# Kernel tuning notes

Measured on AMD Instinct MI355X. Metric: run time of the kernel, lower is better.

## Reference

```python
import jax, jax.numpy as jnp
import numpy as np

TOL = 1e-4
MAX_ITER = 50


def _newton_fixed_point(W, x):
    """Solve z = tanh(z @ W.T + x) by Newton's method (batched).

    W: [U, U], x: [B, U]. Returns (out=tanh(z*@W.T+x), z*).
    """
    B, U = x.shape
    I = jnp.eye(U, dtype=x.dtype)

    def cond(carry):
        _, it, err = carry
        return (it < MAX_ITER) & (err >= TOL)

    def body(carry):
        z, it, _ = carry
        z_lin = z @ W.T + x                      # [B, U]
        g = z - jnp.tanh(z_lin)                  # residual
        err = jnp.linalg.norm(g)                 # global Frobenius norm (as torch.norm)
        sech2 = 1.0 / jnp.cosh(z_lin) ** 2       # [B, U]
        J = I[None, :, :] - sech2[:, :, None] * W[None, :, :]  # [B, U, U]
        dz = jnp.linalg.solve(J, g[:, :, None])[:, :, 0]
        # torch breaks BEFORE the update when err < tol; emulate with where
        z_new = jnp.where(err < TOL, z, z - dz)
        return (z_new, it + 1, err)

    z0 = jnp.tanh(x)
    init = (z0, jnp.array(0, jnp.int32), jnp.array(jnp.inf, x.dtype))
    z_star, _, _ = jax.lax.while_loop(cond, body, init)
    out = jnp.tanh(z_star @ W.T + x)
    return out, z_star


def setup_inputs() -> dict:
    key = jax.random.key(0)
    ks = jax.random.split(key, 6)
    B, D_IN, U, D_OUT, L = 2048, 784, 128, 10, 2
    x = jax.random.normal(ks[0], (B, D_IN), dtype=jnp.float32)
    Wi = jax.random.normal(ks[1], (U, D_IN), dtype=jnp.float32) * (1.0 / np.sqrt(D_IN))
    bi = jax.random.normal(ks[2], (U,), dtype=jnp.float32) * 0.01
    # contractive block weights (like nn.Linear init scale) so Newton converges
    Wb = jax.random.normal(ks[3], (L, U, U), dtype=jnp.float32) * (0.5 / np.sqrt(U))
    Wo = jax.random.normal(ks[4], (D_OUT, U), dtype=jnp.float32) * (1.0 / np.sqrt(U))
    bo = jax.random.normal(ks[5], (D_OUT,), dtype=jnp.float32) * 0.01
    return {"x": x, "Wi": Wi, "bi": bi, "Wb": Wb, "Wo": Wo, "bo": bo}


def reference(x, Wi, bi, Wb, Wo, bo):
    z = x @ Wi.T + bi                              # input linear
    for l in range(Wb.shape[0]):                   # implicit Newton blocks
        z, _ = _newton_fixed_point(Wb[l], z)
    logits = z @ Wo.T + bo                         # output linear
    return jax.nn.softmax(logits, axis=1)
```

## Files before the change

### kernel.cpp

```cpp
#include <hip/hip_runtime.h>
#include <math.h>

#define U 128
#define NIT 10

typedef __attribute__((ext_vector_type(8))) short bf16x8;
typedef __attribute__((ext_vector_type(4))) float f32x4;
typedef __attribute__((ext_vector_type(4))) unsigned int u32x4;

__device__ inline unsigned int pack2(float a, float b) {
    return (__float_as_uint(a) >> 16) | (__float_as_uint(b) & 0xFFFF0000u);
}
__device__ inline float lo_of(float a) {
    return a - __uint_as_float(__float_as_uint(a) & 0xFFFF0000u);
}
__device__ inline unsigned int packrn(float a, float b) {
    unsigned int r;
    asm("v_cvt_pk_bf16_f32 %0, %1, %2" : "=v"(r) : "v"(a), "v"(b));
    return r;
}
__device__ inline float fromhi(unsigned short h) {
    return __uint_as_float(((unsigned int)h) << 16);
}
__device__ inline float rcp_fast(float x) {
    float r;
    asm("v_rcp_f32 %0, %1" : "=v"(r) : "v"(x));
    return r;
}
__device__ inline float tanh_fast(float v) {
    float e = __expf(2.0f * v);
    return __builtin_fmaf(-2.0f, rcp_fast(e + 1.0f), 1.0f);
}
#define MFMA(A, B, C) __builtin_amdgcn_mfma_f32_16x16x32_bf16(A, B, C, 0, 0, 0)

#define SPLIT8(P4, Q4, H, LO)                                              \
{   u32x4 h_, l_;                                                          \
    h_[0] = pack2(P4.x, P4.y); h_[1] = pack2(P4.z, P4.w);                  \
    h_[2] = pack2(Q4.x, Q4.y); h_[3] = pack2(Q4.z, Q4.w);                  \
    l_[0] = pack2(lo_of(P4.x), lo_of(P4.y));                               \
    l_[1] = pack2(lo_of(P4.z), lo_of(P4.w));                               \
    l_[2] = pack2(lo_of(Q4.x), lo_of(Q4.y));                               \
    l_[3] = pack2(lo_of(Q4.z), lo_of(Q4.w));                               \
    H  = __builtin_bit_cast(bf16x8, h_);                                   \
    LO = __builtin_bit_cast(bf16x8, l_); }

__global__ __launch_bounds__(512) void k_gemm_in(
        const float* __restrict__ X, const float* __restrict__ Wi,
        const float* __restrict__ bi, float* __restrict__ zA) {
    __shared__ f32x4 redS[4][64];
    const int tid  = threadIdx.x;
    const int w    = tid >> 6;
    const int lane = tid & 63;
    const int l15  = lane & 15;
    const int lq   = lane >> 4;
    const int slab = blockIdx.x & 127;
    const int ch   = blockIdx.x >> 7;
    const int ct   = w & 3;
    const int kh   = w >> 2;
    const int r0   = slab * 16;
    const int cb   = ch * 64 + ct * 16;
    const int colA = cb + l15;
    const int KD   = 784;

    const float* xp = &X[(long)(r0 + l15) * KD];
    const float* wp = &Wi[(long)colA * KD];

    f32x4 a0 = {0.f, 0.f, 0.f, 0.f};
    f32x4 a1 = {0.f, 0.f, 0.f, 0.f};
    f32x4 a2 = {0.f, 0.f, 0.f, 0.f};
    if (kh == 0) {
        float4 b4 = *(const float4*)&bi[cb + lq * 4];
        a0[0] = b4.x; a0[1] = b4.y; a0[2] = b4.z; a0[3] = b4.w;
    }

    const int kbase = kh ? 384 : 0;
    #pragma unroll 6
    for (int c = 0; c < 12; ++c) {
        const int k = kbase + c * 32 + lq * 8;
        float4 xa = *(const float4*)&xp[k];
        float4 xb = *(const float4*)&xp[k + 4];
        float4 wa = *(const float4*)&wp[k];
        float4 wb = *(const float4*)&wp[k + 4];
        bf16x8 ah, al, bh, bl;
        SPLIT8(xa, xb, ah, al)
        SPLIT8(wa, wb, bh, bl)
        a0 = MFMA(bh, ah, a0);
        a1 = MFMA(bh, al, a1);
        a2 = MFMA(bl, ah, a2);
    }
    if (kh) {
        float4 z4 = make_float4(0.f, 0.f, 0.f, 0.f);
        float4 xa = z4, xb = z4, wa = z4, wb = z4;
        if (lq < 2) {
            const int k = 768 + lq * 8;
            xa = *(const float4*)&xp[k];
            xb = *(const float4*)&xp[k + 4];
            wa = *(const float4*)&wp[k];
            wb = *(const float4*)&wp[k + 4];
        }
        bf16x8 ah, al, bh, bl;
        SPLIT8(xa, xb, ah, al)
        SPLIT8(wa, wb, bh, bl)
        a0 = MFMA(bh, ah, a0);
        a1 = MFMA(bh, al, a1);
        a2 = MFMA(bl, ah, a2);
    }

    f32x4 r;
    #pragma unroll
    for (int i = 0; i < 4; ++i) r[i] = a0[i] + a1[i] + a2[i];

    if (kh) redS[ct][lane] = r;
    __syncthreads();
    if (!kh) {
        f32x4 o = redS[ct][lane];
        float4 st;
        st.x = r[0] + o[0]; st.y = r[1] + o[1];
        st.z = r[2] + o[2]; st.w = r[3] + o[3];
        *(float4*)&zA[(long)(r0 + l15) * U + cb + lq * 4] = st;
    }
}

__global__ __launch_bounds__(256) void k_picard(
        const float* __restrict__ zA, const float* __restrict__ Wb,
        const float* __restrict__ Wo, const float* __restrict__ bo,
        float* __restrict__ Out, int L) {
    __shared__ unsigned short zhS[2][16 * U];

    const int tid  = threadIdx.x;
    const int w    = tid >> 6;
    const int lane = tid & 63;
    const int l15  = lane & 15;
    const int lq   = lane >> 4;
    const int r0   = blockIdx.x * 16;

    float xf[8], zr[8];
    {
        const float* zrow = &zA[(long)(r0 + l15) * U + w * 32 + lq * 4];
        float4 x40 = *(const float4*)&zrow[0];
        float4 x41 = *(const float4*)&zrow[16];
        xf[0] = x40.x; xf[1] = x40.y; xf[2] = x40.z; xf[3] = x40.w;
        xf[4] = x41.x; xf[5] = x41.y; xf[6] = x41.z; xf[7] = x41.w;
    }

    const int swz = (l15 & 7) << 4;
    int offA[4];
    #pragma unroll
    for (int ks = 0; ks < 4; ++ks)
        offA[ks] = l15 * 256 + ((64 * ks + 16 * lq) ^ swz);
    const int offW0 = l15 * 256 + (((64 * w + 8 * lq)) ^ swz);
    const int offW1 = l15 * 256 + (((64 * w + 32 + 8 * lq)) ^ swz);

    char* zhB = (char*)&zhS[0][0];

    for (int l = 0; l < L; ++l) {
        bf16x8 whf[2][4];
        #pragma unroll
        for (int ct = 0; ct < 2; ++ct) {
            const int colA = w * 32 + ct * 16 + l15;
            const float* wrow = &Wb[((long)l * U + colA) * U];
            #pragma unroll
            for (int ks = 0; ks < 4; ++ks) {
                const int k = ks * 32 + lq * 8;
                float4 p = *(const float4*)&wrow[k];
                float4 q = *(const float4*)&wrow[k + 4];
                u32x4 h;
                h[0] = packrn(p.x, p.y); h[1] = packrn(p.z, p.w);
                h[2] = packrn(q.x, q.y); h[3] = packrn(q.z, q.w);
                whf[ct][ks] = __builtin_bit_cast(bf16x8, h);
            }
        }

        {
            uint2 h0, h1;
            #pragma unroll
            for (int i = 0; i < 8; ++i) zr[i] = tanh_fast(xf[i]);
            h0.x = packrn(zr[0], zr[1]); h0.y = packrn(zr[2], zr[3]);
            h1.x = packrn(zr[4], zr[5]); h1.y = packrn(zr[6], zr[7]);
            *(uint2*)(zhB + offW0) = h0;
            *(uint2*)(zhB + offW1) = h1;
        }
        __syncthreads();

        #pragma unroll 2
        for (int it = 0; it < NIT; ++it) {
            const int cur = it & 1;
            const int nxt = cur ^ 1;
            bf16x8 zhf[4];
            #pragma unroll
            for (int ks = 0; ks < 4; ++ks)
                zhf[ks] = *(const bf16x8*)(zhB + cur * 4096 + offA[ks]);

            f32x4 A0 = {xf[0], xf[1], xf[2], xf[3]};
            f32x4 Z4 = {0.f, 0.f, 0.f, 0.f};
            f32x4 A1 = Z4;
            f32x4 B0 = {xf[4], xf[5], xf[6], xf[7]};
            f32x4 B1 = Z4;
            A0 = MFMA(whf[0][0], zhf[0], A0);
            B0 = MFMA(whf[1][0], zhf[0], B0);
            A1 = MFMA(whf[0][2], zhf[2], A1);
            B1 = MFMA(whf[1][2], zhf[2], B1);
            A0 = MFMA(whf[0][1], zhf[1], A0);
            B0 = MFMA(whf[1][1], zhf[1], B0);
            A1 = MFMA(whf[0][3], zhf[3], A1);
            B1 = MFMA(whf[1][3], zhf[3], B1);

            #pragma unroll
            for (int i = 0; i < 4; ++i) {
                zr[i]     = tanh_fast(A0[i] + A1[i]);
                zr[4 + i] = tanh_fast(B0[i] + B1[i]);
            }
            uint2 h0, h1;
            h0.x = packrn(zr[0], zr[1]); h0.y = packrn(zr[2], zr[3]);
            h1.x = packrn(zr[4], zr[5]); h1.y = packrn(zr[6], zr[7]);
            *(uint2*)(zhB + nxt * 4096 + offW0) = h0;
            *(uint2*)(zhB + nxt * 4096 + offW1) = h1;
            __syncthreads();
        }

        {
            bf16x8 zhf[4];
            #pragma unroll
            for (int ks = 0; ks < 4; ++ks)
                zhf[ks] = *(const bf16x8*)(zhB + offA[ks]);
            #pragma unroll
            for (int ct = 0; ct < 2; ++ct) {
                const int colA = w * 32 + ct * 16 + l15;
                const float* wrow = &Wb[((long)l * U + colA) * U];
                f32x4 dH = {xf[ct * 4 + 0], xf[ct * 4 + 1],
                            xf[ct * 4 + 2], xf[ct * 4 + 3]};
                f32x4 dL = {0.f, 0.f, 0.f, 0.f};
                #pragma unroll
                for (int ks = 0; ks < 4; ++ks) {
                    const float* wp = &wrow[32 * ks + 8 * lq];
                    float4 p = *(const float4*)&wp[0];
                    float4 q = *(const float4*)&wp[4];
                    u32x4 h = __builtin_bit_cast(u32x4, whf[ct][ks]);
                    float lo0 = p.x - __uint_as_float(h[0] << 16);
                    float lo1 = p.y - __uint_as_float(h[0] & 0xFFFF0000u);
                    float lo2 = p.z - __uint_as_float(h[1] << 16);
                    float lo3 = p.w - __uint_as_float(h[1] & 0xFFFF0000u);
                    float lo4 = q.x - __uint_as_float(h[2] << 16);
                    float lo5 = q.y - __uint_as_float(h[2] & 0xFFFF0000u);
                    float lo6 = q.z - __uint_as_float(h[3] << 16);
                    float lo7 = q.w - __uint_as_float(h[3] & 0xFFFF0000u);
                    u32x4 lw;
                    lw[0] = packrn(lo0, lo1); lw[1] = packrn(lo2, lo3);
                    lw[2] = packrn(lo4, lo5); lw[3] = packrn(lo6, lo7);
                    bf16x8 wlf = __builtin_bit_cast(bf16x8, lw);
                    dH = MFMA(whf[ct][ks], zhf[ks], dH);
                    dL = MFMA(wlf, zhf[ks], dL);
                }
                #pragma unroll
                for (int i = 0; i < 4; ++i)
                    xf[ct * 4 + i] = tanh_fast(dH[i] + dL[i]);
            }
        }
        __syncthreads();
    }

    {
        unsigned int h0 = packrn(xf[0], xf[1]);
        unsigned int h1 = packrn(xf[2], xf[3]);
        unsigned int h2 = packrn(xf[4], xf[5]);
        unsigned int h3 = packrn(xf[6], xf[7]);
        uint2 H0, H1, L0, L1;
        H0.x = h0; H0.y = h1; H1.x = h2; H1.y = h3;
        L0.x = packrn(xf[0] - __uint_as_float(h0 << 16),
                      xf[1] - __uint_as_float(h0 & 0xFFFF0000u));
        L0.y = packrn(xf[2] - __uint_as_float(h1 << 16),
                      xf[3] - __uint_as_float(h1 & 0xFFFF0000u));
        L1.x = packrn(xf[4] - __uint_as_float(h2 << 16),
                      xf[5] - __uint_as_float(h2 & 0xFFFF0000u));
        L1.y = packrn(xf[6] - __uint_as_float(h3 << 16),
                      xf[7] - __uint_as_float(h3 & 0xFFFF0000u));
        *(uint2*)(zhB + offW0) = H0;
        *(uint2*)(zhB + offW1) = H1;
        *(uint2*)(zhB + 4096 + offW0) = L0;
        *(uint2*)(zhB + 4096 + offW1) = L1;
    }
    __syncthreads();

    if (w == 0) {
        bf16x8 woh[4], wol[4];
        #pragma unroll
        for (int ks = 0; ks < 4; ++ks) {
            float4 p = make_float4(0.f, 0.f, 0.f, 0.f), q = p;
            if (l15 < 10) {
                const float* worow = &Wo[l15 * U + ks * 32 + lq * 8];
                p = *(const float4*)&worow[0];
                q = *(const float4*)&worow[4];
            }
            SPLIT8(p, q, woh[ks], wol[ks])
        }
        bf16x8 zf[4], zl[4];
        #pragma unroll
        for (int ks = 0; ks < 4; ++ks) {
            zf[ks] = *(const bf16x8*)(zhB + offA[ks]);
            zl[ks] = *(const bf16x8*)(zhB + 4096 + offA[ks]);
        }

        f32x4 d0 = {0.f, 0.f, 0.f, 0.f};
        f32x4 d1 = d0, d2 = d0;
        #pragma unroll
        for (int ks = 0; ks < 4; ++ks) {
            d0 = MFMA(woh[ks], zf[ks], d0);
            d1 = MFMA(wol[ks], zf[ks], d1);
            d2 = MFMA(woh[ks], zl[ks], d2);
        }
        float lg[4];
        #pragma unroll
        for (int i = 0; i < 4; ++i) {
            const int c = 4 * lq + i;
            lg[i] = (c < 10) ? (d0[i] + d1[i] + d2[i] + bo[c]) : -1e30f;
        }
        float m = fmaxf(fmaxf(lg[0], lg[1]), fmaxf(lg[2], lg[3]));
        m = fmaxf(m, __shfl_xor(m, 16));
        m = fmaxf(m, __shfl_xor(m, 32));
        float e[4], s = 0.f;
        #pragma unroll
        for (int i = 0; i < 4; ++i) { e[i] = __expf(lg[i] - m); s += e[i]; }
        s += __shfl_xor(s, 16);
        s += __shfl_xor(s, 32);
        const float inv = rcp_fast(s);
        const float inv2 = inv * (2.0f - s * inv);
        #pragma unroll
        for (int i = 0; i < 4; ++i) {
            const int c = 4 * lq + i;
            if (c < 10) Out[(long)(r0 + l15) * 10 + c] = e[i] * inv2;
        }
    }
}

extern "C" void kernel_launch(void* const* d_in, const int* in_sizes, int n_in,
                              void* d_out, int out_size, void* d_ws, size_t ws_size,
                              hipStream_t stream) {
    const float* x  = (const float*)d_in[0];
    const float* Wi = (const float*)d_in[1];
    const float* bi = (const float*)d_in[2];
    const float* Wb = (const float*)d_in[3];
    const float* Wo = (const float*)d_in[4];
    const float* bo = (const float*)d_in[5];
    float* out = (float*)d_out;

    const int DIN = 784;
    const int B   = in_sizes[0] / DIN;
    const int L   = in_sizes[3] / (U * U);

    float* zA = (float*)d_ws;

    k_gemm_in<<<256, 512, 0, stream>>>(x, Wi, bi, zA);
    k_picard<<<B / 16, 256, 0, stream>>>(zA, Wb, Wo, bo, out, L);
}
```

Baseline: 31.08 us.

## Process two 16-row batch tiles per block to reuse weight fragments

Each k_picard block now handles 32 batch rows as two independent 16-row tiles. The bf16 weight fragments loaded into registers and the per-iteration barriers are shared across both tiles, and the two independent MFMA chains can interleave. This halves the grid to 64 blocks. On a GPU with many CUs that means fewer active CUs, so per-block latency roughly doubles while total weight loading drops.

Result: slower. 36.81 us (+18.4%).

```diff
diff --git a/kernel.cpp b/kernel.cpp
--- a/kernel.cpp
+++ b/kernel.cpp
@@ -18,9 +18,6 @@
     unsigned int r;
     asm("v_cvt_pk_bf16_f32 %0, %1, %2" : "=v"(r) : "v"(a), "v"(b));
     return r;
-}
-__device__ inline float fromhi(unsigned short h) {
-    return __uint_as_float(((unsigned int)h) << 16);
 }
 __device__ inline float rcp_fast(float x) {
     float r;
@@ -125,22 +122,27 @@
         const float* __restrict__ zA, const float* __restrict__ Wb,
         const float* __restrict__ Wo, const float* __restrict__ bo,
         float* __restrict__ Out, int L) {
-    __shared__ unsigned short zhS[2][16 * U];
+    __shared__ unsigned short zhS[2][2][16 * U];
 
     const int tid  = threadIdx.x;
     const int w    = tid >> 6;
     const int lane = tid & 63;
     const int l15  = lane & 15;
     const int lq   = lane >> 4;
-    const int r0   = blockIdx.x * 16;
-
-    float xf[8], zr[8];
+    const int r0   = blockIdx.x * 32;
+
+    float xf0[8], xf1[8], zr[8];
     {
-        const float* zrow = &zA[(long)(r0 + l15) * U + w * 32 + lq * 4];
-        float4 x40 = *(const float4*)&zrow[0];
-        float4 x41 = *(const float4*)&zrow[16];
-        xf[0] = x40.x; xf[1] = x40.y; xf[2] = x40.z; xf[3] = x40.w;
-        xf[4] = x41.x; xf[5] = x41.y; xf[6] = x41.z; xf[7] = x41.w;
+        const float* zr0 = &zA[(long)(r0 + l15) * U + w * 32 + lq * 4];
+        const float* zr1 = &zA[(long)(r0 + 16 + l15) * U + w * 32 + lq * 4];
+        float4 a = *(const float4*)&zr0[0];
+        float4 b = *(const float4*)&zr0[16];
+        float4 c = *(const float4*)&zr1[0];
+        float4 d = *(const float4*)&zr1[16];
+        xf0[0]=a.x; xf0[1]=a.y; xf0[2]=a.z; xf0[3]=a.w;
+        xf0[4]=b.x; xf0[5]=b.y; xf0[6]=b.z; xf0[7]=b.w;
+        xf1[0]=c.x; xf1[1]=c.y; xf1[2]=c.z; xf1[3]=c.w;
+        xf1[4]=d.x; xf1[5]=d.y; xf1[6]=d.z; xf1[7]=d.w;
     }
 
     const int swz = (l15 & 7) << 4;
@@ -151,7 +153,8 @@
     const int offW0 = l15 * 256 + (((64 * w + 8 * lq)) ^ swz);
     const int offW1 = l15 * 256 + (((64 * w + 32 + 8 * lq)) ^ swz);
 
-    char* zhB = (char*)&zhS[0][0];
+    char* zB0 = (char*)&zhS[0][0][0];
+    char* zB1 = (char*)&zhS[1][0][0];
 
     for (int l = 0; l < L; ++l) {
         bf16x8 whf[2][4];
@@ -174,11 +177,17 @@
         {
             uint2 h0, h1;
             #pragma unroll
-            for (int i = 0; i < 8; ++i) zr[i] = tanh_fast(xf[i]);
+            for (int i = 0; i < 8; ++i) zr[i] = tanh_fast(xf0[i]);
             h0.x = packrn(zr[0], zr[1]); h0.y = packrn(zr[2], zr[3]);
             h1.x = packrn(zr[4], zr[5]); h1.y = packrn(zr[6], zr[7]);
-            *(uint2*)(zhB + offW0) = h0;
-            *(uint2*)(zhB + offW1) = h1;
+            *(uint2*)(zB0 + offW0) = h0;
+            *(uint2*)(zB0 + offW1) = h1;
+            #pragma unroll
+            for (int i = 0; i < 8; ++i) zr[i] = tanh_fast(xf1[i]);
+            h0.x = packrn(zr[0], zr[1]); h0.y = packrn(zr[2], zr[3]);
+            h1.x = packrn(zr[4], zr[5]); h1.y = packrn(zr[6], zr[7]);
+            *(uint2*)(zB1 + offW0) = h0;
+            *(uint2*)(zB1 + offW1) = h1;
         }
         __syncthreads();
 
@@ -186,50 +195,76 @@
         for (int it = 0; it < NIT; ++it) {
             const int cur = it & 1;
             const int nxt = cur ^ 1;
-            bf16x8 zhf[4];
-            #pragma unroll
-            for (int ks = 0; ks < 4; ++ks)
-                zhf[ks] = *(const bf16x8*)(zhB + cur * 4096 + offA[ks]);
-
-            f32x4 A0 = {xf[0], xf[1], xf[2], xf[3]};
+            bf16x8 z0f[4], z1f[4];
+            #pragma unroll
+            for (int ks = 0; ks < 4; ++ks) {
+                z0f[ks] = *(const bf16x8*)(zB0 + cur * 4096 + offA[ks]);
+                z1f[ks] = *(const bf16x8*)(zB1 + cur * 4096 + offA[ks]);
+            }
+
             f32x4 Z4 = {0.f, 0.f, 0.f, 0.f};
+            f32x4 A0 = {xf0[0], xf0[1], xf0[2], xf0[3]};
             f32x4 A1 = Z4;
-            f32x4 B0 = {xf[4], xf[5], xf[6], xf[7]};
+            f32x4 B0 = {xf0[4], xf0[5], xf0[6], xf0[7]};
             f32x4 B1 = Z4;
-            A0 = MFMA(whf[0][0], zhf[0], A0);
-            B0 = MFMA(whf[1][0], zhf[0], B0);
-            A1 = MFMA(whf[0][2], zhf[2], A1);
-            B1 = MFMA(whf[1][2], zhf[2], B1);
-            A0 = MFMA(whf[0][1], zhf[1], A0);
-            B0 = MFMA(whf[1][1], zhf[1], B0);
-            A1 = MFMA(whf[0][3], zhf[3], A1);
-            B1 = MFMA(whf[1][3], zhf[3], B1);
-
+            f32x4 C0 = {xf1[0], xf1[1], xf1[2], xf1[3]};
+            f32x4 C1 = Z4;
+            f32x4 D0 = {xf1[4], xf1[5], xf1[6], xf1[7]};
+            f32x4 D1 = Z4;
+            A0 = MFMA(whf[0][0], z0f[0], A0);
+            C0 = MFMA(whf[0][0], z1f[0], C0);
+            B0 = MFMA(whf[1][0], z0f[0], B0);
+            D0 = MFMA(whf[1][0], z1f[0], D0);
+            A1 = MFMA(whf[0][2], z0f[2], A1);
+            C1 = MFMA(whf[0][2], z1f[2], C1);
+            B1 = MFMA(whf[1][2], z0f[2], B1);
+            D1 = MFMA(whf[1][2], z1f[2], D1);
+            A0 = MFMA(whf[0][1], z0f[1], A0);
+            C0 = MFMA(whf[0][1], z1f[1], C0);
+            B0 = MFMA(whf[1][1], z0f[1], B0);
+            D0 = MFMA(whf[1][1], z1f[1], D0);
+            A1 = MFMA(whf[0][3], z0f[3], A1);
+            C1 = MFMA(whf[0][3], z1f[3], C1);
+            B1 = MFMA(whf[1][3], z0f[3], B1);
+            D1 = MFMA(whf[1][3], z1f[3], D1);
+
+            uint2 h0, h1;
             #pragma unroll
             for (int i = 0; i < 4; ++i) {
                 zr[i]     = tanh_fast(A0[i] + A1[i]);
                 zr[4 + i] = tanh_fast(B0[i] + B1[i]);
             }
-            uint2 h0, h1;
             h0.x = packrn(zr[0], zr[1]); h0.y = packrn(zr[2], zr[3]);
             h1.x = packrn(zr[4], zr[5]); h1.y = packrn(zr[6], zr[7]);
-            *(uint2*)(zhB + nxt * 4096 + offW0) = h0;
-            *(uint2*)(zhB + nxt * 4096 + offW1) = h1;
+            *(uint2*)(zB0 + nxt * 4096 + offW0) = h0;
+            *(uint2*)(zB0 + nxt * 4096 + offW1) = h1;
+            #pragma unroll
+            for (int i = 0; i < 4; ++i) {
+                zr[i]     = tanh_fast(C0[i] + C1[i]);
+                zr[4 + i] = tanh_fast(D0[i] + D1[i]);
+            }
+            h0.x = packrn(zr[0], zr[1]); h0.y = packrn(zr[2], zr[3]);
+            h1.x = packrn(zr[4], zr[5]); h1.y = packrn(zr[6], zr[7]);
+            *(uint2*)(zB1 + nxt * 4096 + offW0) = h0;
+            *(uint2*)(zB1 + nxt * 4096 + offW1) = h1;
             __syncthreads();
         }
 
         {
-            bf16x8 zhf[4];
-            #pragma unroll
-            for (int ks = 0; ks < 4; ++ks)
-                zhf[ks] = *(const bf16x8*)(zhB + offA[ks]);
+            bf16x8 z0f[4], z1f[4];
+            #pragma unroll
+            for (int ks = 0; ks < 4; ++ks) {
+                z0f[ks] = *(const bf16x8*)(zB0 + offA[ks]);
+                z1f[ks] = *(const bf16x8*)(zB1 + offA[ks]);
+            }
             #pragma unroll
             for (int ct = 0; ct < 2; ++ct) {
                 const int colA = w * 32 + ct * 16 + l15;
                 const float* wrow = &Wb[((long)l * U + colA) * U];
-                f32x4 dH = {xf[ct * 4 + 0], xf[ct * 4 + 1],
-                            xf[ct * 4 + 2], xf[ct * 4 + 3]};
-                f32x4 dL = {0.f, 0.f, 0.f, 0.f};
+                f32x4 dH0 = {xf0[ct*4+0], xf0[ct*4+1], xf0[ct*4+2], xf0[ct*4+3]};
+                f32x4 dH1 = {xf1[ct*4+0], xf1[ct*4+1], xf1[ct*4+2], xf1[ct*4+3]};
+                f32x4 dL0 = {0.f, 0.f, 0.f, 0.f};
+                f32x4 dL1 = dL0;
                 #pragma unroll
                 for (int ks = 0; ks < 4; ++ks) {
                     const float* wp = &wrow[32 * ks + 8 * lq];
@@ -248,40 +283,50 @@
                     lw[0] = packrn(lo0, lo1); lw[1] = packrn(lo2, lo3);
                     lw[2] = packrn(lo4, lo5); lw[3] = packrn(lo6, lo7);
                     bf16x8 wlf = __builtin_bit_cast(bf16x8, lw);
-                    dH = MFMA(whf[ct][ks], zhf[ks], dH);
-                    dL = MFMA(wlf, zhf[ks], dL);
+                    dH0 = MFMA(whf[ct][ks], z0f[ks], dH0);
+                    dH1 = MFMA(whf[ct][ks], z1f[ks], dH1);
+                    dL0 = MFMA(wlf, z0f[ks], dL0);
+                    dL1 = MFMA(wlf, z1f[ks], dL1);
                 }
                 #pragma unroll
-                for (int i = 0; i < 4; ++i)
-                    xf[ct * 4 + i] = tanh_fast(dH[i] + dL[i]);
+                for (int i = 0; i < 4; ++i) {
+                    xf0[ct*4+i] = tanh_fast(dH0[i] + dL0[i]);
+                    xf1[ct*4+i] = tanh_fast(dH1[i] + dL1[i]);
+                }
             }
         }
         __syncthreads();
     }
 
     {
-        unsigned int h0 = packrn(xf[0], xf[1]);
-        unsigned int h1 = packrn(xf[2], xf[3]);
-        unsigned int h2 = packrn(xf[4], xf[5]);
-        unsigned int h3 = packrn(xf[6], xf[7]);
-        uint2 H0, H1, L0, L1;
-        H0.x = h0; H0.y = h1; H1.x = h2; H1.y = h3;
-        L0.x = packrn(xf[0] - __uint_as_float(h0 << 16),
-                      xf[1] - __uint_as_float(h0 & 0xFFFF0000u));
-        L0.y = packrn(xf[2] - __uint_as_float(h1 << 16),
-                      xf[3] - __uint_as_float(h1 & 0xFFFF0000u));
-        L1.x = packrn(xf[4] - __uint_as_float(h2 << 16),
-                      xf[5] - __uint_as_float(h2 & 0xFFFF0000u));
-        L1.y = packrn(xf[6] - __uint_as_float(h3 << 16),
-                      xf[7] - __uint_as_float(h3 & 0xFFFF0000u));
-        *(uint2*)(zhB + offW0) = H0;
-        *(uint2*)(zhB + offW1) = H1;
-        *(uint2*)(zhB + 4096 + offW0) = L0;
-        *(uint2*)(zhB + 4096 + offW1) = L1;
+        #pragma unroll
+        for (int t = 0; t < 2; ++t) {
+            const float* xs = t ? xf1 : xf0;
+            char* zb = t ? zB1 : zB0;
+            unsigned int h0 = packrn(xs[0], xs[1]);
+            unsigned int h1 = packrn(xs[2], xs[3]);
+            unsigned int h2 = packrn(xs[4], xs[5]);
+            unsigned int h3 = packrn(xs[6], xs[7]);
+            uint2 H0, H1, L0, L1;
+            H0.x = h0; H0.y = h1; H1.x = h2; H1.y = h3;
+            L0.x = packrn(xs[0] - __uint_as_float(h0 << 16),
+                          xs[1] - __uint_as_float(h0 & 0xFFFF0000u));
+            L0.y = packrn(xs[2] - __uint_as_float(h1 << 16),
+                          xs[3] - __uint_as_float(h1 & 0xFFFF0000u));
+            L1.x = packrn(xs[4] - __uint_as_float(h2 << 16),
+                          xs[5] - __uint_as_float(h2 & 0xFFFF0000u));
+            L1.y = packrn(xs[6] - __uint_as_float(h3 << 16),
+                          xs[7] - __uint_as_float(h3 & 0xFFFF0000u));
+            *(uint2*)(zb + offW0) = H0;
+            *(uint2*)(zb + offW1) = H1;
+            *(uint2*)(zb + 4096 + offW0) = L0;
+            *(uint2*)(zb + 4096 + offW1) = L1;
+        }
     }
     __syncthreads();
 
-    if (w == 0) {
+    if (w < 2) {
+        char* zb = w ? zB1 : zB0;
         bf16x8 woh[4], wol[4];
         #pragma unroll
         for (int ks = 0; ks < 4; ++ks) {
@@ -296,8 +341,8 @@
         bf16x8 zf[4], zl[4];
         #pragma unroll
         for (int ks = 0; ks < 4; ++ks) {
-            zf[ks] = *(const bf16x8*)(zhB + offA[ks]);
-            zl[ks] = *(const bf16x8*)(zhB + 4096 + offA[ks]);
+            zf[ks] = *(const bf16x8*)(zb + offA[ks]);
+            zl[ks] = *(const bf16x8*)(zb + 4096 + offA[ks]);
         }
 
         f32x4 d0 = {0.f, 0.f, 0.f, 0.f};
@@ -327,7 +372,7 @@
         #pragma unroll
         for (int i = 0; i < 4; ++i) {
             const int c = 4 * lq + i;
-            if (c < 10) Out[(long)(r0 + l15) * 10 + c] = e[i] * inv2;
+            if (c < 10) Out[(long)(r0 + w * 16 + l15) * 10 + c] = e[i] * inv2;
         }
     }
 }
@@ -350,5 +395,5 @@
     float* zA = (float*)d_ws;
 
     k_gemm_in<<<256, 512, 0, stream>>>(x, Wi, bi, zA);
-    k_picard<<<B / 16, 256, 0, stream>>>(zA, Wb, Wo, bo, out, L);
-}
+    k_picard<<<B / 32, 256, 0, stream>>>(zA, Wb, Wo, bo, out, L);
+}
```
